# Performance work log

Hardware: AMD Instinct MI355X
Metric: run time of the kernel (lower is better)

The kernel has to match this reference:

```python
import jax, jax.numpy as jnp
import numpy as np

H = 512   # hidden_size
L = 2     # decoder_layer
B = 64    # batch
T = 2048  # encoder sequence length


def setup_inputs() -> dict:
    key = jax.random.key(0)
    ks = jax.random.split(key, 9)
    hidden = jax.random.normal(ks[0], (L, B, H), dtype=jnp.float32)
    encoder_output = jax.random.normal(ks[1], (T, B, H), dtype=jnp.float32)
    enc_len = jax.random.randint(ks[2], (B,), T // 2, T + 1, dtype=jnp.int32)
    s = 0.02
    Wh = jax.random.normal(ks[3], (H, H), dtype=jnp.float32) * s  # hidden_proj
    bh = jnp.zeros((H,), dtype=jnp.float32)
    We = jax.random.normal(ks[4], (H, H), dtype=jnp.float32) * s  # encoder_output_proj
    be = jnp.zeros((H,), dtype=jnp.float32)
    Wo = jax.random.normal(ks[5], (H,), dtype=jnp.float32) * s    # out: Linear(H, 1)
    bo = jnp.zeros((1,), dtype=jnp.float32)
    return {"hidden": hidden, "encoder_output": encoder_output, "enc_len": enc_len,
            "Wh": Wh, "bh": bh, "We": We, "be": be, "Wo": Wo, "bo": bo}


def reference(hidden, encoder_output, enc_len, Wh, bh, We, be, Wo, bo):
    # encoder_output: [T,B,H] -> [B,T,H]
    enc = jnp.swapaxes(encoder_output, 0, 1)
    # bmm with (1/L) addMask == mean over decoder layers: [L,B,H] -> [B,H]
    h = jnp.mean(hidden, axis=0)
    hidden_attn = h @ Wh.T + bh                      # [B,H]
    enc_attn = jnp.einsum('bth,oh->bto', enc, We) + be  # [B,T,H]
    res = jnp.tanh(enc_attn + hidden_attn[:, None, :])  # [B,T,H]
    scores = res @ Wo + bo[0]                        # [B,T]
    # per-sample masked softmax over valid prefix [0:enc_len[i])
    mask = jnp.arange(T)[None, :] < enc_len[:, None]  # [B,T]
    neg = jnp.asarray(-jnp.inf, dtype=scores.dtype)
    w = jax.nn.softmax(jnp.where(mask, scores, neg), axis=1)
    w = jnp.where(mask, w, 0.0)
    return w[:, :, None]  # [B,T,1]
```

## Files before the change

### kernel.cpp

```cpp
#include <hip/hip_runtime.h>
#include <stdint.h>


typedef __attribute__((ext_vector_type(4))) float f32x4;
typedef __attribute__((ext_vector_type(8))) __bf16 bf16x8;
typedef __attribute__((ext_vector_type(8))) unsigned short u16x8;
typedef __attribute__((ext_vector_type(4))) unsigned short u16x4;

#define AS3 __attribute__((address_space(3)))
#define AS1 __attribute__((address_space(1)))

__device__ __forceinline__ unsigned short f2bf(float f) {
  unsigned u = __builtin_bit_cast(unsigned, f);
  return (unsigned short)((u + 0x7FFFu + ((u >> 16) & 1u)) >> 16);
}

__device__ __forceinline__ float fast_tanh(float x) {
  float t = __expf(-2.0f * __builtin_fabsf(x));
  float r = (1.0f - t) * __builtin_amdgcn_rcpf(1.0f + t);
  return __builtin_copysignf(r, x);
}

__global__ void prep_comb_kernel(const float* __restrict__ hidden,
                                 const float* __restrict__ Wh,
                                 const float* __restrict__ bh,
                                 const float* __restrict__ be,
                                 float* __restrict__ comb) {
  __shared__ float hb[512];
  const int b = blockIdx.x, tid = threadIdx.x;
  for (int i = tid; i < 512; i += 256)
    hb[i] = 0.5f * (hidden[b * 512 + i] + hidden[32768 + b * 512 + i]);
  __syncthreads();
  for (int o = tid; o < 512; o += 256) {
    const f32x4* wr = (const f32x4*)(Wh + o * 512);
    const f32x4* hv = (const f32x4*)hb;
    float s = 0.f;
    for (int k = 0; k < 128; ++k) {
      f32x4 w = wr[k], x = hv[k];
      s += w.x * x.x + w.y * x.y + w.z * x.z + w.w * x.w;
    }
    comb[b * 512 + o] = s + bh[o] + be[o];
  }
}

__global__ void prep_pack_kernel(const float* __restrict__ We,
                                 unsigned short* __restrict__ wsw) {
  const int gid = blockIdx.x * 256 + threadIdx.x;
  const int s = gid >> 11;
  const int rem = gid & 2047;
  const int o = rem >> 2;
  const int g = rem & 3;
  const float* src = We + o * 512 + s * 32 + g * 8;
  u16x8 p;
#pragma unroll
  for (int e = 0; e < 8; ++e) p[e] = f2bf(src[e]);
  const int dgran = s * 2048 + o * 4 + ((g ^ (o >> 1)) & 3);
  *(u16x8*)(wsw + (long)dgran * 8) = p;
}

__global__ __launch_bounds__(512, 4) void gemm_score_kernel(
    const float* __restrict__ enc,
    const unsigned short* __restrict__ wsw,
    const float* __restrict__ comb,
    const float* __restrict__ Wo,
    float* __restrict__ scores)
{
  __shared__ __align__(16) unsigned char Blds[2][32768];
  __shared__ __align__(16) unsigned char Alds[2][4096];
  __shared__ float spart[4][64];

  const int tid = threadIdx.x;
  const int lane = tid & 63;
  const int wave = tid >> 6;
  const int wm = wave >> 2;
  const int wn = wave & 3;
  const int l15 = lane & 15;
  const int lq = lane >> 4;

  const long r0 = (long)blockIdx.x * 64;

  const int arow = tid >> 3;
  const int ac4 = tid & 7;
  const float* aglb = enc + (r0 + arow) * 512 + ac4 * 4;
  const unsigned awoff = (unsigned)(arow * 64 +
                         ((((ac4 >> 1) ^ (arow >> 1)) & 3) << 4) + (ac4 & 1) * 8);

  const unsigned char* bglb = (const unsigned char*)wsw + (long)tid * 16;

  const unsigned swz = (unsigned)(((lq ^ (l15 >> 1)) & 3) << 4);
  const unsigned aoff = (unsigned)((wm * 32 + l15) * 64) + swz;
  const unsigned boff = (unsigned)((wn * 128 + l15) * 64) + swz;

  f32x4 acc[2][8];
#pragma unroll
  for (int m = 0; m < 2; ++m)
#pragma unroll
    for (int j = 0; j < 8; ++j) acc[m][j] = (f32x4){0.f, 0.f, 0.f, 0.f};

  f32x4 av = *(const f32x4*)aglb;
#pragma unroll
  for (int c = 0; c < 4; ++c)
    __builtin_amdgcn_global_load_lds((const AS1 unsigned int*)(bglb + c * 8192),
                                     (AS3 unsigned int*)(&Blds[0][tid * 16 + c * 8192]),
                                     16, 0, 0);
  {
    u16x4 p;
    p[0] = f2bf(av.x); p[1] = f2bf(av.y); p[2] = f2bf(av.z); p[3] = f2bf(av.w);
    *(u16x4*)(&Alds[0][awoff]) = p;
  }
  __syncthreads();

  for (int ks = 0; ks < 16; ++ks) {
    const int cur = ks & 1;
    if (ks < 15) {
      const unsigned char* bs = bglb + (long)(ks + 1) * 32768;
#pragma unroll
      for (int c = 0; c < 4; ++c)
        __builtin_amdgcn_global_load_lds((const AS1 unsigned int*)(bs + c * 8192),
                                         (AS3 unsigned int*)(&Blds[cur ^ 1][tid * 16 + c * 8192]),
                                         16, 0, 0);
      av = *(const f32x4*)(aglb + (ks + 1) * 32);
    }

    bf16x8 af0 = *(const bf16x8*)(&Alds[cur][aoff]);
    bf16x8 af1 = *(const bf16x8*)(&Alds[cur][aoff + 1024]);
#pragma unroll
    for (int jn = 0; jn < 8; ++jn) {
      bf16x8 bf = *(const bf16x8*)(&Blds[cur][boff + jn * 1024]);
      acc[0][jn] = __builtin_amdgcn_mfma_f32_16x16x32_bf16(af0, bf, acc[0][jn], 0, 0, 0);
      acc[1][jn] = __builtin_amdgcn_mfma_f32_16x16x32_bf16(af1, bf, acc[1][jn], 0, 0, 0);
    }

    if (ks < 15) {
      u16x4 p;
      p[0] = f2bf(av.x); p[1] = f2bf(av.y); p[2] = f2bf(av.z); p[3] = f2bf(av.w);
      *(u16x4*)(&Alds[cur ^ 1][awoff]) = p;
    }
    __syncthreads();
  }

  float wo[8];
#pragma unroll
  for (int jn = 0; jn < 8; ++jn) wo[jn] = Wo[wn * 128 + jn * 16 + l15];

  float ps[2][4];
#pragma unroll
  for (int m = 0; m < 2; ++m) {
#pragma unroll
    for (int q = 0; q < 4; ++q) {
      const int row = wm * 32 + m * 16 + lq * 4 + q;
      const float* crow = comb + row * 512;
      float s = 0.f;
#pragma unroll
      for (int jn = 0; jn < 8; ++jn) {
        const int col = wn * 128 + jn * 16 + l15;
        const float x = acc[m][jn][q] + crow[col];
        s += fast_tanh(x) * wo[jn];
      }
      ps[m][q] = s;
    }
  }
#pragma unroll
  for (int m = 0; m < 2; ++m)
#pragma unroll
    for (int q = 0; q < 4; ++q) {
      float s = ps[m][q];
      s += __shfl_xor(s, 1, 16);
      s += __shfl_xor(s, 2, 16);
      s += __shfl_xor(s, 4, 16);
      s += __shfl_xor(s, 8, 16);
      if (l15 == 0) spart[wn][wm * 32 + m * 16 + lq * 4 + q] = s;
    }
  __syncthreads();
  if (tid < 64) {
    float s = spart[0][tid] + spart[1][tid] + spart[2][tid] + spart[3][tid];
    scores[(long)tid * 2048 + blockIdx.x] = s;
  }
}

__global__ void softmax_kernel(const float* __restrict__ scores,
                               const int* __restrict__ enc_len,
                               float* __restrict__ out) {
  const int b = blockIdx.x;
  const int tid = threadIdx.x;
  const int lane = tid & 63;
  const int wv = tid >> 6;
  __shared__ float red[4];
  const int n = enc_len[b];
  const float* sc = scores + (long)b * 2048;

  float v[8];
  float m = -1e30f;
#pragma unroll
  for (int j = 0; j < 8; ++j) {
    const int t = tid + j * 256;
    v[j] = sc[t];
    if (t < n) m = fmaxf(m, v[j]);
  }
#pragma unroll
  for (int k = 32; k; k >>= 1) m = fmaxf(m, __shfl_xor(m, k, 64));
  if (lane == 0) red[wv] = m;
  __syncthreads();
  m = fmaxf(fmaxf(red[0], red[1]), fmaxf(red[2], red[3]));
  __syncthreads();

  float s = 0.f;
#pragma unroll
  for (int j = 0; j < 8; ++j) {
    const int t = tid + j * 256;
    const float e = (t < n) ? __expf(v[j] - m) : 0.f;
    v[j] = e;
    s += e;
  }
#pragma unroll
  for (int k = 32; k; k >>= 1) s += __shfl_xor(s, k, 64);
  if (lane == 0) red[wv] = s;
  __syncthreads();
  s = red[0] + red[1] + red[2] + red[3];
  const float inv = 1.0f / s;
#pragma unroll
  for (int j = 0; j < 8; ++j) {
    const int t = tid + j * 256;
    out[(long)b * 2048 + t] = v[j] * inv;
  }
}

extern "C" void kernel_launch(void* const* d_in, const int* in_sizes, int n_in,
                              void* d_out, int out_size, void* d_ws, size_t ws_size,
                              hipStream_t stream) {
  const float* hidden = (const float*)d_in[0];
  const float* enc    = (const float*)d_in[1];
  const int*   enclen = (const int*)d_in[2];
  const float* Wh     = (const float*)d_in[3];
  const float* bh     = (const float*)d_in[4];
  const float* We     = (const float*)d_in[5];
  const float* be     = (const float*)d_in[6];
  const float* Wo     = (const float*)d_in[7];
  float* out = (float*)d_out;

  uint8_t* ws = (uint8_t*)d_ws;
  unsigned short* wsw = (unsigned short*)ws;
  float* comb   = (float*)(ws + 524288);
  float* scores = (float*)(ws + 524288 + 131072);

  hipLaunchKernelGGL(prep_comb_kernel, dim3(64), dim3(256), 0, stream,
                     hidden, Wh, bh, be, comb);
  hipLaunchKernelGGL(prep_pack_kernel, dim3(128), dim3(256), 0, stream, We, wsw);
  hipLaunchKernelGGL(gemm_score_kernel, dim3(2048), dim3(512), 0, stream,
                     enc, wsw, comb, Wo, scores);
  hipLaunchKernelGGL(softmax_kernel, dim3(64), dim3(256), 0, stream,
                     scores, enclen, out);
}
```

Measured before the change: 184.5 us.

## Double GEMM row tile per block with triple-buffered B and deeper prefetch

The fused projection-plus-score kernel now processes 128 encoder rows per block (two timesteps) instead of 64. Each B fragment read from LDS therefore feeds four MFMAs instead of two, and the grid is halved. The weight tiles are triple-buffered in LDS and the A (encoder) loads are prefetched two k-steps ahead, using 8-element bf16 packs. A lighter barrier that waits only on LDS counters replaces __syncthreads. The cost is much higher LDS use and more accumulator registers, which lowers occupancy. The barrier also relies on in-order vector-memory completion to make sure the async LDS loads have landed.

New measurement: 152.1 us. 17.5% less time.

```diff
diff --git a/kernel.cpp b/kernel.cpp
--- a/kernel.cpp
+++ b/kernel.cpp
@@ -5,7 +5,6 @@
 typedef __attribute__((ext_vector_type(4))) float f32x4;
 typedef __attribute__((ext_vector_type(8))) __bf16 bf16x8;
 typedef __attribute__((ext_vector_type(8))) unsigned short u16x8;
-typedef __attribute__((ext_vector_type(4))) unsigned short u16x4;
 
 #define AS3 __attribute__((address_space(3)))
 #define AS1 __attribute__((address_space(1)))
@@ -20,6 +19,12 @@
   float r = (1.0f - t) * __builtin_amdgcn_rcpf(1.0f + t);
   return __builtin_copysignf(r, x);
 }
+
+#define WAVE_SYNC() do { \
+  asm volatile("s_waitcnt lgkmcnt(0)" ::: "memory"); \
+  __builtin_amdgcn_s_barrier(); \
+  __builtin_amdgcn_sched_barrier(0); \
+} while (0)
 
 __global__ void prep_comb_kernel(const float* __restrict__ hidden,
                                  const float* __restrict__ Wh,
@@ -58,16 +63,16 @@
   *(u16x8*)(wsw + (long)dgran * 8) = p;
 }
 
-__global__ __launch_bounds__(512, 4) void gemm_score_kernel(
+__global__ __launch_bounds__(512, 2) void gemm_score_kernel(
     const float* __restrict__ enc,
     const unsigned short* __restrict__ wsw,
     const float* __restrict__ comb,
     const float* __restrict__ Wo,
     float* __restrict__ scores)
 {
-  __shared__ __align__(16) unsigned char Blds[2][32768];
-  __shared__ __align__(16) unsigned char Alds[2][4096];
-  __shared__ float spart[4][64];
+  __shared__ __align__(16) unsigned char Blds[3][32768];
+  __shared__ __align__(16) unsigned char Alds[2][8192];
+  __shared__ float spart[4][128];
 
   const int tid = threadIdx.x;
   const int lane = tid & 63;
@@ -77,79 +82,98 @@
   const int l15 = lane & 15;
   const int lq = lane >> 4;
 
-  const long r0 = (long)blockIdx.x * 64;
-
-  const int arow = tid >> 3;
-  const int ac4 = tid & 7;
-  const float* aglb = enc + (r0 + arow) * 512 + ac4 * 4;
-  const unsigned awoff = (unsigned)(arow * 64 +
-                         ((((ac4 >> 1) ^ (arow >> 1)) & 3) << 4) + (ac4 & 1) * 8);
+  const long r0 = (long)blockIdx.x * 128;
+
+  const int arow = tid >> 2;
+  const int ag = tid & 3;
+  const float* aglb = enc + (r0 + arow) * 512 + ag * 8;
+  const unsigned awoff = (unsigned)(arow * 64 + (((ag ^ (arow >> 1)) & 3) << 4));
 
   const unsigned char* bglb = (const unsigned char*)wsw + (long)tid * 16;
 
   const unsigned swz = (unsigned)(((lq ^ (l15 >> 1)) & 3) << 4);
-  const unsigned aoff = (unsigned)((wm * 32 + l15) * 64) + swz;
+  const unsigned aoff = (unsigned)((wm * 64 + l15) * 64) + swz;
   const unsigned boff = (unsigned)((wn * 128 + l15) * 64) + swz;
 
-  f32x4 acc[2][8];
-#pragma unroll
-  for (int m = 0; m < 2; ++m)
+  f32x4 acc[4][8];
+#pragma unroll
+  for (int m = 0; m < 4; ++m)
 #pragma unroll
     for (int j = 0; j < 8; ++j) acc[m][j] = (f32x4){0.f, 0.f, 0.f, 0.f};
 
-  f32x4 av = *(const f32x4*)aglb;
+  f32x4 apre[2][2];
+
 #pragma unroll
   for (int c = 0; c < 4; ++c)
     __builtin_amdgcn_global_load_lds((const AS1 unsigned int*)(bglb + c * 8192),
                                      (AS3 unsigned int*)(&Blds[0][tid * 16 + c * 8192]),
                                      16, 0, 0);
+  apre[0][0] = *(const f32x4*)(aglb);
+  apre[0][1] = *(const f32x4*)(aglb + 4);
+#pragma unroll
+  for (int c = 0; c < 4; ++c)
+    __builtin_amdgcn_global_load_lds((const AS1 unsigned int*)(bglb + 32768 + c * 8192),
+                                     (AS3 unsigned int*)(&Blds[1][tid * 16 + c * 8192]),
+                                     16, 0, 0);
+  apre[1][0] = *(const f32x4*)(aglb + 32);
+  apre[1][1] = *(const f32x4*)(aglb + 32 + 4);
   {
-    u16x4 p;
-    p[0] = f2bf(av.x); p[1] = f2bf(av.y); p[2] = f2bf(av.z); p[3] = f2bf(av.w);
-    *(u16x4*)(&Alds[0][awoff]) = p;
-  }
-  __syncthreads();
-
+    u16x8 p;
+    p[0] = f2bf(apre[0][0].x); p[1] = f2bf(apre[0][0].y);
+    p[2] = f2bf(apre[0][0].z); p[3] = f2bf(apre[0][0].w);
+    p[4] = f2bf(apre[0][1].x); p[5] = f2bf(apre[0][1].y);
+    p[6] = f2bf(apre[0][1].z); p[7] = f2bf(apre[0][1].w);
+    *(u16x8*)(&Alds[0][awoff]) = p;
+  }
+  WAVE_SYNC();
+
+#pragma unroll
   for (int ks = 0; ks < 16; ++ks) {
-    const int cur = ks & 1;
-    if (ks < 15) {
-      const unsigned char* bs = bglb + (long)(ks + 1) * 32768;
+    if (ks + 2 < 16) {
+      const unsigned char* bs = bglb + (long)(ks + 2) * 32768;
+      unsigned char* bd = &Blds[(ks + 2) % 3][tid * 16];
 #pragma unroll
       for (int c = 0; c < 4; ++c)
         __builtin_amdgcn_global_load_lds((const AS1 unsigned int*)(bs + c * 8192),
-                                         (AS3 unsigned int*)(&Blds[cur ^ 1][tid * 16 + c * 8192]),
+                                         (AS3 unsigned int*)(bd + c * 8192),
                                          16, 0, 0);
-      av = *(const f32x4*)(aglb + (ks + 1) * 32);
-    }
-
-    bf16x8 af0 = *(const bf16x8*)(&Alds[cur][aoff]);
-    bf16x8 af1 = *(const bf16x8*)(&Alds[cur][aoff + 1024]);
+      apre[ks & 1][0] = *(const f32x4*)(aglb + (ks + 2) * 32);
+      apre[ks & 1][1] = *(const f32x4*)(aglb + (ks + 2) * 32 + 4);
+    }
+    __builtin_amdgcn_sched_barrier(0);
+
+    bf16x8 af[4];
+#pragma unroll
+    for (int m = 0; m < 4; ++m)
+      af[m] = *(const bf16x8*)(&Alds[ks & 1][aoff + m * 1024]);
 #pragma unroll
     for (int jn = 0; jn < 8; ++jn) {
-      bf16x8 bf = *(const bf16x8*)(&Blds[cur][boff + jn * 1024]);
-      acc[0][jn] = __builtin_amdgcn_mfma_f32_16x16x32_bf16(af0, bf, acc[0][jn], 0, 0, 0);
-      acc[1][jn] = __builtin_amdgcn_mfma_f32_16x16x32_bf16(af1, bf, acc[1][jn], 0, 0, 0);
+      bf16x8 bf = *(const bf16x8*)(&Blds[ks % 3][boff + jn * 1024]);
+#pragma unroll
+      for (int m = 0; m < 4; ++m)
+        acc[m][jn] = __builtin_amdgcn_mfma_f32_16x16x32_bf16(af[m], bf, acc[m][jn], 0, 0, 0);
     }
 
     if (ks < 15) {
-      u16x4 p;
-      p[0] = f2bf(av.x); p[1] = f2bf(av.y); p[2] = f2bf(av.z); p[3] = f2bf(av.w);
-      *(u16x4*)(&Alds[cur ^ 1][awoff]) = p;
-    }
-    __syncthreads();
+      const f32x4* a = apre[(ks + 1) & 1];
+      u16x8 p;
+      p[0] = f2bf(a[0].x); p[1] = f2bf(a[0].y); p[2] = f2bf(a[0].z); p[3] = f2bf(a[0].w);
+      p[4] = f2bf(a[1].x); p[5] = f2bf(a[1].y); p[6] = f2bf(a[1].z); p[7] = f2bf(a[1].w);
+      *(u16x8*)(&Alds[(ks + 1) & 1][awoff]) = p;
+    }
+    WAVE_SYNC();
   }
 
   float wo[8];
 #pragma unroll
   for (int jn = 0; jn < 8; ++jn) wo[jn] = Wo[wn * 128 + jn * 16 + l15];
 
-  float ps[2][4];
-#pragma unroll
-  for (int m = 0; m < 2; ++m) {
+#pragma unroll
+  for (int m = 0; m < 4; ++m) {
 #pragma unroll
     for (int q = 0; q < 4; ++q) {
-      const int row = wm * 32 + m * 16 + lq * 4 + q;
-      const float* crow = comb + row * 512;
+      const int b = m * 16 + lq * 4 + q;
+      const float* crow = comb + b * 512;
       float s = 0.f;
 #pragma unroll
       for (int jn = 0; jn < 8; ++jn) {
@@ -157,24 +181,19 @@
         const float x = acc[m][jn][q] + crow[col];
         s += fast_tanh(x) * wo[jn];
       }
-      ps[m][q] = s;
-    }
-  }
-#pragma unroll
-  for (int m = 0; m < 2; ++m)
-#pragma unroll
-    for (int q = 0; q < 4; ++q) {
-      float s = ps[m][q];
       s += __shfl_xor(s, 1, 16);
       s += __shfl_xor(s, 2, 16);
       s += __shfl_xor(s, 4, 16);
       s += __shfl_xor(s, 8, 16);
-      if (l15 == 0) spart[wn][wm * 32 + m * 16 + lq * 4 + q] = s;
-    }
-  __syncthreads();
-  if (tid < 64) {
+      if (l15 == 0) spart[wn][wm * 64 + b] = s;
+    }
+  }
+  __syncthreads();
+  if (tid < 128) {
     float s = spart[0][tid] + spart[1][tid] + spart[2][tid] + spart[3][tid];
-    scores[(long)tid * 2048 + blockIdx.x] = s;
+    const int b = tid & 63;
+    const long t = (long)blockIdx.x * 2 + (tid >> 6);
+    scores[(long)b * 2048 + t] = s;
   }
 }
 
@@ -246,7 +265,7 @@
   hipLaunchKernelGGL(prep_comb_kernel, dim3(64), dim3(256), 0, stream,
                      hidden, Wh, bh, be, comb);
   hipLaunchKernelGGL(prep_pack_kernel, dim3(128), dim3(256), 0, stream, We, wsw);
-  hipLaunchKernelGGL(gemm_score_kernel, dim3(2048), dim3(512), 0, stream,
+  hipLaunchKernelGGL(gemm_score_kernel, dim3(1024), dim3(512), 0, stream,
                      enc, wsw, comb, Wo, scores);
   hipLaunchKernelGGL(softmax_kernel, dim3(64), dim3(256), 0, stream,
                      scores, enclen, out);
```
